# Kernel tuning notes

Measured on AMD Instinct MI355X. Metric: run time of the kernel, lower is better.

The kernel has to match this reference:

```python
import jax, jax.numpy as jnp
import numpy as np

WINDOW = 16
VD = 6
HID = 16


def setup_inputs() -> dict:
    key = jax.random.key(0)
    ks = jax.random.split(key, 10)
    B, S = 256, 4096
    sc = 0.1
    return {
        "x": jax.random.normal(ks[0], (B, S, 2), jnp.float32),
        "h_0": jnp.zeros((B, HID), jnp.float32),
        "fir_I_w": jax.random.normal(ks[1], (VD, WINDOW), jnp.float32) * sc,
        "fir_Q_w": jax.random.normal(ks[2], (VD, WINDOW), jnp.float32) * sc,
        "W_fi_w": jax.random.normal(ks[3], (HID, 2 * VD), jnp.float32) * sc,
        "W_fi_b": jnp.zeros((HID,), jnp.float32),
        "W_fh_w": jax.random.normal(ks[4], (HID, HID), jnp.float32) * sc,
        "W_gi_w": jax.random.normal(ks[5], (HID, 2 * VD), jnp.float32) * sc,
        "W_gi_b": jnp.zeros((HID,), jnp.float32),
        "W_gh_w": jax.random.normal(ks[6], (HID, HID), jnp.float32) * sc,
        "W_out_I_w": jax.random.normal(ks[7], (1, HID), jnp.float32) * sc,
        "W_out_I_b": jnp.zeros((1,), jnp.float32),
        "W_out_Q_w": jax.random.normal(ks[8], (1, HID), jnp.float32) * sc,
        "W_out_Q_b": jnp.zeros((1,), jnp.float32),
    }


def _tile_theta(t, hidden):
    # pr_block replication logic for vd_units < hidden <= 3*vd_units cases
    if VD >= hidden:
        return t[..., :hidden]
    elif hidden <= 2 * VD:
        return jnp.concatenate([t, t[..., : hidden - VD]], axis=-1)
    else:
        return jnp.concatenate([t, t, t[..., : hidden - 2 * VD]], axis=-1)


def reference(x, h_0, fir_I_w, fir_Q_w, W_fi_w, W_fi_b, W_fh_w,
              W_gi_w, W_gi_b, W_gh_w, W_out_I_w, W_out_I_b,
              W_out_Q_w, W_out_Q_b):
    B, S, _ = x.shape
    # Causal sliding windows: window at t covers x[t-15 .. t] with zero pad.
    xp = jnp.concatenate([jnp.zeros((B, WINDOW - 1, 2), x.dtype), x], axis=1)
    idx = jnp.arange(S)[:, None] + jnp.arange(WINDOW)[None, :]  # (S, W)
    win = xp[:, idx, :]  # (B, S, W, 2)
    wI, wQ = win[..., 0], win[..., 1]  # (B, S, W)
    # Complex FIR filter
    I_fir = jnp.einsum('bsw,vw->bsv', wI, fir_I_w) - jnp.einsum('bsw,vw->bsv', wQ, fir_Q_w)
    Q_fir = jnp.einsum('bsw,vw->bsv', wI, fir_Q_w) + jnp.einsum('bsw,vw->bsv', wQ, fir_I_w)
    mag = jnp.sqrt(I_fir * I_fir + Q_fir * Q_fir) + 1e-8
    mag2 = mag * mag
    sin_t = Q_fir / mag
    cos_t = I_fir / mag
    # L = stack([mag, mag2], dim=2).view(B, S, 2*VD)
    L = jnp.stack([mag, mag2], axis=2).reshape(B, S, 2 * VD)
    # Precompute input contributions to gates; scan the recurrence.
    fi = jnp.einsum('bsl,hl->bsh', L, W_fi_w) + W_fi_b  # (B,S,H)
    gi = jnp.einsum('bsl,hl->bsh', L, W_gi_w) + W_gi_b

    def step(h, inp):
        fi_t, gi_t = inp
        f = jax.nn.sigmoid(fi_t + h @ W_fh_w.T)
        g = jnp.tanh(gi_t + h @ W_gh_w.T)
        h = f * h + (1.0 - f) * g
        return h, h

    _, h_seq = jax.lax.scan(step, h_0, (fi.transpose(1, 0, 2), gi.transpose(1, 0, 2)))
    h_seq = h_seq.transpose(1, 0, 2)  # (B, S, H)
    hidden = h_seq.shape[-1]
    cos_r = _tile_theta(cos_t, hidden)
    sin_r = _tile_theta(sin_t, hidden)
    I_rot = h_seq * cos_r
    Q_rot = h_seq * sin_r
    oI = I_rot @ W_out_I_w.T + W_out_I_b  # (B,S,1)
    oQ = Q_rot @ W_out_Q_w.T + W_out_Q_b
    out_I = oI - oQ
    out_Q = oQ + oI
    return jnp.concatenate([out_I, out_Q], axis=-1)
```

## Files before the change

### kernel.cpp

```cpp
#include <hip/hip_runtime.h>
#include <stdint.h>

#define DEV __device__ __forceinline__

constexpr int Bb   = 256;
constexpr int Ss   = 4096;
constexpr int HIDN = 16;
constexpr int VDN  = 6;
constexpr int WINN = 16;

constexpr int BPG   = 32;
constexpr int NG    = Bb / BPG;
constexpr int CHUNK = 16;
constexpr int WARM  = 16;
constexpr int NCH   = Ss / CHUNK;
constexpr int NPH   = (CHUNK + WARM) / 4;
constexpr int EPH   = WARM / 4;

constexpr size_t WSL_BYTES = (size_t)NG * Ss * BPG * 16;
constexpr size_t WSC_BYTES = (size_t)NG * Ss * BPG * 24;

typedef __fp16 h2v   __attribute__((ext_vector_type(2)));
typedef __fp16 f16x8 __attribute__((ext_vector_type(8)));
typedef float  f32x16 __attribute__((ext_vector_type(16)));

DEV uint32_t pk16(float a, float b) {
    h2v t = __builtin_amdgcn_cvt_pkrtz(a, b);
    uint32_t u; __builtin_memcpy(&u, &t, 4); return u;
}
DEV void up16(uint32_t u, float& a, float& b) {
    h2v t; __builtin_memcpy(&t, &u, 4);
    a = (float)t[0]; b = (float)t[1];
}
DEV uint32_t sqpk(uint32_t u) {
    h2v t; __builtin_memcpy(&t, &u, 4);
    t = t * t;
    uint32_t r; __builtin_memcpy(&r, &t, 4); return r;
}
DEV f32x16 MF(const uint32_t* a, const uint32_t* b, f32x16 c) {
    f16x8 av, bv;
    __builtin_memcpy(&av, a, 16);
    __builtin_memcpy(&bv, b, 16);
    return __builtin_amdgcn_mfma_f32_32x32x16_f16(av, bv, c, 0, 0, 0);
}

template<int C> DEV int   dpp_i(int v)  { return __builtin_amdgcn_update_dpp(0, v, C, 0xF, 0xF, false); }
template<int C> DEV float dpp_f(float v){ return __int_as_float(dpp_i<C>(__float_as_int(v))); }
#define DPP_ALL(X) X(1,0x121) X(2,0x122) X(3,0x123) X(4,0x124) X(5,0x125) X(6,0x126) X(7,0x127) \
  X(8,0x128) X(9,0x129) X(10,0x12A) X(11,0x12B) X(12,0x12C) X(13,0x12D) X(14,0x12E) X(15,0x12F)

__global__ __launch_bounds__(256, 4) void boja_front(
    const float* __restrict__ x,
    const float* __restrict__ fIw, const float* __restrict__ fQw,
    uint4* __restrict__ wsl, uint2* __restrict__ wsc)
{
    __shared__ __align__(16) uint4 lsl[256];
    const int tid = threadIdx.x;
    const int tq  = tid & 7;
    const int b_  = tid >> 3;
    const int G   = blockIdx.y;
    const int t0  = blockIdx.x * 8;
    const int t   = t0 + tq;
    const int b   = G * BPG + b_;
    const int id  = b * Ss + t;
    const float2* x2 = (const float2*)x;

    float wI[WINN], wQ[WINN];
    if (t >= WINN - 1) {
#pragma unroll
        for (int w = 0; w < WINN; ++w) { float2 v = x2[id - 15 + w]; wI[w] = v.x; wQ[w] = v.y; }
    } else {
#pragma unroll
        for (int w = 0; w < WINN; ++w) {
            int ts = t - 15 + w;
            float2 v = (ts >= 0) ? x2[id - 15 + w] : make_float2(0.f, 0.f);
            wI[w] = v.x; wQ[w] = v.y;
        }
    }
    float aI[VDN], aQ[VDN];
#pragma unroll
    for (int v = 0; v < VDN; ++v) { aI[v] = 0.f; aQ[v] = 0.f; }
#pragma unroll
    for (int w = 0; w < WINN; ++w) {
#pragma unroll
        for (int v = 0; v < VDN; ++v) {
            aI[v] = fmaf( wI[w], fIw[v*16+w], aI[v]);
            aI[v] = fmaf(-wQ[w], fQw[v*16+w], aI[v]);
            aQ[v] = fmaf( wI[w], fQw[v*16+w], aQ[v]);
            aQ[v] = fmaf( wQ[w], fIw[v*16+w], aQ[v]);
        }
    }
    float mg[VDN];
    uint32_t sc[VDN];
#pragma unroll
    for (int v = 0; v < VDN; ++v) {
        float m2 = fmaf(aI[v], aI[v], aQ[v]*aQ[v]);
        mg[v] = __builtin_amdgcn_sqrtf(m2) + 1e-8f;
        float iv = __builtin_amdgcn_rcpf(mg[v]);
        sc[v] = pk16(aI[v]*iv, aQ[v]*iv);
    }
    {
        const size_t cb = ((size_t)(G * Ss + t) * BPG + b_) * 3;
        wsc[cb+0] = make_uint2(sc[0], sc[1]);
        wsc[cb+1] = make_uint2(sc[2], sc[3]);
        wsc[cb+2] = make_uint2(sc[4], sc[5]);
    }
    lsl[tq*32 + b_] = make_uint4(pk16(mg[0], mg[1]), pk16(mg[2], mg[3]),
                                 pk16(mg[4], mg[5]), pk16(mg[0]*mg[0], mg[1]*mg[1]));
    __syncthreads();
    {
        const int tq2 = tid >> 5, b2 = tid & 31;
        wsl[((size_t)(G*Ss + t0 + tq2)) * BPG + b2] = lsl[tid];
    }
}

__global__ __launch_bounds__(64, 2) void boja_rnn(
    const uint4* __restrict__ wsl, const uint2* __restrict__ wsc,
    const float* __restrict__ h0,
    const float* __restrict__ Wfh, const float* __restrict__ Wgh,
    const float* __restrict__ Wfi, const float* __restrict__ bfi,
    const float* __restrict__ Wgi, const float* __restrict__ bgi,
    const float* __restrict__ WoI, const float* __restrict__ boI,
    const float* __restrict__ WoQ, const float* __restrict__ boQ,
    float* __restrict__ out)
{
    const int l  = threadIdx.x;
    const int b_ = l & 31;
    const int h_ = l >> 5;
    const int G  = blockIdx.x & (NG - 1);
    const int ci = blockIdx.x >> 3;

    const int t_out0  = ci * CHUNK;
    const int t_start = t_out0 - WARM;
    const bool useh0  = (t_start <= 0);

    const float CF = -1.4426950408889634f;
    const float CG =  2.8853900817779268f;
    const int   m  = b_;
    const float sA = (m < 16) ? CF : CG;

    uint32_t a1[4], a2[4];
#pragma unroll
    for (int d = 0; d < 4; ++d) {
        float wv[2], uv[2];
#pragma unroll
        for (int q = 0; q < 2; ++q) {
            const int e = d*2 + q;
            const int k = (e & 3) + 8*(e >> 2) + 4*h_;
            wv[q] = ((m < 16) ? Wfh[m*16 + k] : Wgh[(m-16)*16 + k]) * sA;
            float u;
            if (k < 12)       u = ((m < 16) ? Wfi[m*12 + k] : Wgi[(m-16)*12 + k]) * sA;
            else if (k == 12) u = ((m < 16) ? bfi[m] : bgi[m-16]) * sA;
            else              u = 0.0f;
            uv[q] = u;
        }
        a1[d] = pk16(wv[0], wv[1]);
        a2[d] = pk16(uv[0], uv[1]);
    }

    float woi[8], woq[8];
#pragma unroll
    for (int r = 0; r < 8; ++r) {
        const int j = (r & 3) + 8*(r >> 2) + 4*h_;
        woi[r] = WoI[j]; woq[r] = WoQ[j];
    }
    const float bo_i = boI[0], bo_q = boQ[0];

    float h0r[8];
    if (useh0) {
        const float* hp = h0 + (size_t)(G*BPG + b_) * HIDN;
        float4 p = *(const float4*)(hp + 4*h_);
        float4 q = *(const float4*)(hp + 8 + 4*h_);
        h0r[0]=p.x; h0r[1]=p.y; h0r[2]=p.z; h0r[3]=p.w;
        h0r[4]=q.x; h0r[5]=q.y; h0r[6]=q.z; h0r[7]=q.w;
    }
    float hreg[8];
#pragma unroll
    for (int r = 0; r < 8; ++r) hreg[r] = 0.0f;
    uint32_t b1[4];
    b1[0]=0u; b1[1]=0u; b1[2]=0u; b1[3]=0u;

    f32x16 zero16;
#pragma unroll
    for (int i = 0; i < 16; ++i) zero16[i] = 0.0f;

    const uint4* lp = wsl + (size_t)G * Ss * BPG + b_;
    const uint2* cp = wsc + ((size_t)G * Ss * BPG + b_) * 3;
    float2* outp = (float2*)out + (size_t)(G*BPG + b_) * Ss;

    uint4 LB[3][4];
    uint2 CB[2][4][3];

    auto loadL = [&](uint4 (&B)[4], int tb) {
#pragma unroll
        for (int s = 0; s < 4; ++s) {
            int tq2 = tb + s; tq2 = (tq2 < 0) ? 0 : tq2;
            B[s] = lp[(size_t)tq2 * BPG];
        }
    };
    auto loadC = [&](uint2 (&C)[4][3], int tb) {
#pragma unroll
        for (int s = 0; s < 4; ++s)
#pragma unroll
            for (int k = 0; k < 3; ++k)
                C[s][k] = cp[(size_t)(tb + s) * (BPG*3) + k];
    };

    loadL(LB[0], t_start);
    loadL(LB[1], t_start + 4);

#define PHASE(P) { \
    const int tb = t_start + 4*(P); \
    if ((P) + 2 < NPH) loadL(LB[((P)+2)%3], t_start + 4*((P)+2)); \
    if ((P) + 1 >= EPH && (P) + 1 < NPH) loadC(CB[((P)+1)&1], t_start + 4*((P)+1)); \
    float ob[8]; \
    uint32_t fw[4][4]; \
    _Pragma("unroll") \
    for (int s = 0; s < 4; ++s) { \
        uint4 v = LB[(P)%3][s]; \
        fw[s][0] = h_ ? v.z : v.x; \
        fw[s][1] = h_ ? v.w : v.y; \
        fw[s][2] = h_ ? 0x00003C00u : sqpk(v.y); \
        fw[s][3] = h_ ? 0u : sqpk(v.z); \
    } \
    f32x16 accL = MF(a2, fw[0], zero16); \
    _Pragma("unroll") \
    for (int s = 0; s < 4; ++s) { \
        if (useh0 && tb + s == 0) { \
            _Pragma("unroll") for (int r = 0; r < 8; ++r) hreg[r] = h0r[r]; \
            b1[0]=pk16(hreg[0],hreg[1]); b1[1]=pk16(hreg[2],hreg[3]); \
            b1[2]=pk16(hreg[4],hreg[5]); b1[3]=pk16(hreg[6],hreg[7]); \
        } \
        f32x16 acc = MF(a1, b1, accL); \
        if (s < 3) accL = MF(a2, fw[s+1], zero16); \
        _Pragma("unroll") \
        for (int r = 0; r < 8; ++r) { \
            float f = __builtin_amdgcn_rcpf(1.0f + __builtin_amdgcn_exp2f(acc[r])); \
            float g = fmaf(-2.0f, __builtin_amdgcn_rcpf(1.0f + __builtin_amdgcn_exp2f(acc[r+8])), 1.0f); \
            hreg[r] = fmaf(f, hreg[r] - g, g); \
        } \
        b1[0]=pk16(hreg[0],hreg[1]); b1[1]=pk16(hreg[2],hreg[3]); \
        b1[2]=pk16(hreg[4],hreg[5]); b1[3]=pk16(hreg[6],hreg[7]); \
        if ((P) >= EPH) { \
            float cs6[6], sn6[6]; \
            up16(CB[(P)&1][s][0].x, cs6[0], sn6[0]); up16(CB[(P)&1][s][0].y, cs6[1], sn6[1]); \
            up16(CB[(P)&1][s][1].x, cs6[2], sn6[2]); up16(CB[(P)&1][s][1].y, cs6[3], sn6[3]); \
            up16(CB[(P)&1][s][2].x, cs6[4], sn6[4]); up16(CB[(P)&1][s][2].y, cs6[5], sn6[5]); \
            float oI = bo_i, oQ = bo_q; \
            const bool hb = (h_ != 0); \
            { \
                float c0,sn0; \
                c0 = hb?cs6[4]:cs6[0]; sn0 = hb?sn6[4]:sn6[0]; oI = fmaf(hreg[0]*c0, woi[0], oI); oQ = fmaf(hreg[0]*sn0, woq[0], oQ); \
                c0 = hb?cs6[5]:cs6[1]; sn0 = hb?sn6[5]:sn6[1]; oI = fmaf(hreg[1]*c0, woi[1], oI); oQ = fmaf(hreg[1]*sn0, woq[1], oQ); \
                c0 = hb?cs6[0]:cs6[2]; sn0 = hb?sn6[0]:sn6[2]; oI = fmaf(hreg[2]*c0, woi[2], oI); oQ = fmaf(hreg[2]*sn0, woq[2], oQ); \
                c0 = hb?cs6[1]:cs6[3]; sn0 = hb?sn6[1]:sn6[3]; oI = fmaf(hreg[3]*c0, woi[3], oI); oQ = fmaf(hreg[3]*sn0, woq[3], oQ); \
                c0 = hb?cs6[0]:cs6[2]; sn0 = hb?sn6[0]:sn6[2]; oI = fmaf(hreg[4]*c0, woi[4], oI); oQ = fmaf(hreg[4]*sn0, woq[4], oQ); \
                c0 = hb?cs6[1]:cs6[3]; sn0 = hb?sn6[1]:sn6[3]; oI = fmaf(hreg[5]*c0, woi[5], oI); oQ = fmaf(hreg[5]*sn0, woq[5], oQ); \
                c0 = hb?cs6[2]:cs6[4]; sn0 = hb?sn6[2]:sn6[4]; oI = fmaf(hreg[6]*c0, woi[6], oI); oQ = fmaf(hreg[6]*sn0, woq[6], oQ); \
                c0 = hb?cs6[3]:cs6[5]; sn0 = hb?sn6[3]:sn6[5]; oI = fmaf(hreg[7]*c0, woi[7], oI); oQ = fmaf(hreg[7]*sn0, woq[7], oQ); \
            } \
            oI += __shfl_xor(oI, 32, 64); \
            oQ += __shfl_xor(oQ, 32, 64); \
            ob[s*2] = oI - oQ; ob[s*2+1] = oI + oQ; \
        } \
    } \
    if ((P) >= EPH && l < 32) { \
        float4* po = (float4*)(outp + tb); \
        po[0] = make_float4(ob[0], ob[1], ob[2], ob[3]); \
        po[1] = make_float4(ob[4], ob[5], ob[6], ob[7]); \
    } \
}

    PHASE(0)  PHASE(1)  PHASE(2)  PHASE(3)
    PHASE(4)  PHASE(5)  PHASE(6)  PHASE(7)
#undef PHASE
}

__global__ __launch_bounds__(64, 2) void bojanet_v2(
    const float* __restrict__ x,   const float* __restrict__ h0,
    const float* __restrict__ fIw, const float* __restrict__ fQw,
    const float* __restrict__ Wfi, const float* __restrict__ bfi,
    const float* __restrict__ Wfh, const float* __restrict__ Wgi,
    const float* __restrict__ bgi, const float* __restrict__ Wgh,
    const float* __restrict__ WoI, const float* __restrict__ boI,
    const float* __restrict__ WoQ, const float* __restrict__ boQ,
    float* __restrict__ out)
{
    constexpr int FCH = 128, FWR = 64, FSB = 16;
    __shared__ __align__(16) float s_fi[FSB * 80];
    __shared__ __align__(16) float s_gi[FSB * 80];
    __shared__ __align__(16) float s_h [FSB * 68];
    __shared__ float s_sc[4 * 12 * 17];

    const int lane = threadIdx.x;
    const int j  = lane & 15;
    const int bl = lane >> 4;
    const int ci = blockIdx.x;
    const int b0 = blockIdx.y * 4;
    const int t_out0  = ci * FCH;
    const int t_start = ci ? (t_out0 - FWR) : 0;
    const int t_end   = t_out0 + FCH;

    int c[16]; c[0] = j;
#define CSET(K,CTL) c[K] = dpp_i<CTL>(j);
    DPP_ALL(CSET)
#undef CSET
    float wf[16], wg[16];
#pragma unroll
    for (int k = 0; k < 16; ++k) { wf[k] = Wfh[j*16 + c[k]]; wg[k] = Wgh[j*16 + c[k]]; }

    float h = (ci == 0) ? h0[(b0 + bl) * HIDN + j] : 0.0f;
    const float2* x2   = (const float2*)x + (size_t)(b0 + bl) * Ss;
    float2*       out2 = (float2*)out     + (size_t)(b0 + bl) * Ss;

    for (int tb = t_start; tb < t_end; tb += FSB) {
        const bool emit = (tb >= t_out0);
        {
            const int tg = tb + j;
            float wI[WINN], wQ[WINN];
            if (tb >= WINN - 1) {
#pragma unroll
                for (int w = 0; w < WINN; ++w) { float2 v = x2[tg - 15 + w]; wI[w] = v.x; wQ[w] = v.y; }
            } else {
#pragma unroll
                for (int w = 0; w < WINN; ++w) {
                    int ts = tg - 15 + w;
                    float2 v = (ts >= 0) ? x2[ts] : make_float2(0.f, 0.f);
                    wI[w] = v.x; wQ[w] = v.y;
                }
            }
            float aI[VDN], aQ[VDN];
#pragma unroll
            for (int v = 0; v < VDN; ++v) { aI[v] = 0.f; aQ[v] = 0.f; }
#pragma unroll
            for (int w = 0; w < WINN; ++w) {
#pragma unroll
                for (int v = 0; v < VDN; ++v) {
                    aI[v] = fmaf( wI[w], fIw[v*16+w], aI[v]);
                    aI[v] = fmaf(-wQ[w], fQw[v*16+w], aI[v]);
                    aQ[v] = fmaf( wI[w], fQw[v*16+w], aQ[v]);
                    aQ[v] = fmaf( wQ[w], fIw[v*16+w], aQ[v]);
                }
            }
            float L[12];
#pragma unroll
            for (int v = 0; v < VDN; ++v) {
                float m2 = fmaf(aI[v], aI[v], aQ[v]*aQ[v]);
                float mg = __builtin_amdgcn_sqrtf(m2) + 1e-8f;
                L[v] = mg; L[6+v] = mg*mg;
                if (emit) {
                    float iv = __builtin_amdgcn_rcpf(mg);
                    s_sc[(bl*12 + v  )*17 + j] = aI[v] * iv;
                    s_sc[(bl*12 + 6+v)*17 + j] = aQ[v] * iv;
                }
            }
            float fi[16], gi[16];
#pragma unroll
            for (int k = 0; k < 16; ++k) { fi[k] = bfi[k]; gi[k] = bgi[k]; }
#pragma unroll
            for (int ll = 0; ll < 12; ++ll) {
#pragma unroll
                for (int k = 0; k < 16; ++k) {
                    fi[k] = fmaf(L[ll], Wfi[k*12+ll], fi[k]);
                    gi[k] = fmaf(L[ll], Wgi[k*12+ll], gi[k]);
                }
            }
            float* pf = &s_fi[j*80 + bl*20];
            float* pg = &s_gi[j*80 + bl*20];
#pragma unroll
            for (int qq = 0; qq < 4; ++qq) {
                *(float4*)(pf + 4*qq) = make_float4(fi[4*qq], fi[4*qq+1], fi[4*qq+2], fi[4*qq+3]);
                *(float4*)(pg + 4*qq) = make_float4(gi[4*qq], gi[4*qq+1], gi[4*qq+2], gi[4*qq+3]);
            }
        }
        __asm__ volatile("s_waitcnt lgkmcnt(0)" ::: "memory");
        {
            const int rb = bl*20 + j;
            float pf0 = s_fi[rb], pf1 = s_fi[80 + rb];
            float pg0 = s_gi[rb], pg1 = s_gi[80 + rb];
#pragma unroll
            for (int tt = 0; tt < FSB; ++tt) {
                const int nx = (tt + 2 < FSB) ? tt + 2 : FSB - 1;
                float pfn = s_fi[nx*80 + rb];
                float pgn = s_gi[nx*80 + rb];
                float hr[16]; hr[0] = h;
#define HSET(K,CTL) hr[K] = dpp_f<CTL>(h);
                DPP_ALL(HSET)
#undef HSET
                float af0 = pf0, af1 = 0.f, ag0 = pg0, ag1 = 0.f;
#pragma unroll
                for (int k = 0; k < 8; ++k) {
                    af0 = fmaf(wf[k],   hr[k],   af0);
                    ag0 = fmaf(wg[k],   hr[k],   ag0);
                    af1 = fmaf(wf[k+8], hr[k+8], af1);
                    ag1 = fmaf(wg[k+8], hr[k+8], ag1);
                }
                float zf = af0 + af1, zg = ag0 + ag1;
                float f = __builtin_amdgcn_rcpf(1.0f + __builtin_amdgcn_exp2f(zf * -1.4426950408889634f));
                float g = fmaf(-2.0f, __builtin_amdgcn_rcpf(1.0f + __builtin_amdgcn_exp2f(zg * 2.8853900817779268f)), 1.0f);
                h = fmaf(f, h - g, g);
                s_h[tt*68 + bl*16 + j] = h;
                pf0 = pf1; pf1 = pfn; pg0 = pg1; pg1 = pgn;
            }
        }
        __asm__ volatile("s_waitcnt lgkmcnt(0)" ::: "memory");
        if (emit) {
            const int tg = tb + j;
            float hv[16];
#pragma unroll
            for (int qq = 0; qq < 4; ++qq) {
                float4 t4 = *(const float4*)&s_h[j*68 + bl*16 + 4*qq];
                hv[4*qq] = t4.x; hv[4*qq+1] = t4.y; hv[4*qq+2] = t4.z; hv[4*qq+3] = t4.w;
            }
            float cs[12];
#pragma unroll
            for (int k = 0; k < 12; ++k) cs[k] = s_sc[(bl*12 + k)*17 + j];
            float oI = boI[0], oQ = boQ[0];
#pragma unroll
            for (int k = 0; k < 16; ++k) {
                int v = (k < 6) ? k : ((k < 12) ? k - 6 : k - 12);
                oI = fmaf(hv[k]*cs[v],   WoI[k], oI);
                oQ = fmaf(hv[k]*cs[6+v], WoQ[k], oQ);
            }
            out2[tg] = make_float2(oI - oQ, oI + oQ);
        }
        __asm__ volatile("s_waitcnt lgkmcnt(0)" ::: "memory");
    }
}

extern "C" void kernel_launch(void* const* d_in, const int* in_sizes, int n_in,
                              void* d_out, int out_size, void* d_ws, size_t ws_size,
                              hipStream_t stream) {
    const float* x   = (const float*)d_in[0];
    const float* h0  = (const float*)d_in[1];
    const float* fIw = (const float*)d_in[2];
    const float* fQw = (const float*)d_in[3];
    const float* Wfi = (const float*)d_in[4];
    const float* bfi = (const float*)d_in[5];
    const float* Wfh = (const float*)d_in[6];
    const float* Wgi = (const float*)d_in[7];
    const float* bgi = (const float*)d_in[8];
    const float* Wgh = (const float*)d_in[9];
    const float* WoI = (const float*)d_in[10];
    const float* boI = (const float*)d_in[11];
    const float* WoQ = (const float*)d_in[12];
    const float* boQ = (const float*)d_in[13];
    float* out = (float*)d_out;

    if (ws_size >= WSL_BYTES + WSC_BYTES) {
        uint4* wsl = (uint4*)d_ws;
        uint2* wsc = (uint2*)((char*)d_ws + WSL_BYTES);
        boja_front<<<dim3(Ss/8, NG), 256, 0, stream>>>(x, fIw, fQw, wsl, wsc);
        boja_rnn<<<dim3(NG * NCH), 64, 0, stream>>>(
            wsl, wsc, h0, Wfh, Wgh, Wfi, bfi, Wgi, bgi, WoI, boI, WoQ, boQ, out);
    } else {
        bojanet_v2<<<dim3(32, Bb / 4), 64, 0, stream>>>(
            x, h0, fIw, fQw, Wfi, bfi, Wfh, Wgi, bgi, Wgh, WoI, boI, WoQ, boQ, out);
    }
}
```

Baseline: 50.91 us.

## Stage RNN chunk inputs into LDS via async global_load_lds with vmcnt waits

The front kernel's cos/sin workspace layout changes to a planar per-timestep arrangement with three 256-byte planes. The RNN kernel now issues all loads for its chunk up front using global_load_lds DMA into shared memory, replacing the register-based triple/double buffering. Each phase waits on a hand-computed vmcnt before reading from LDS, so compute can start while later loads are still in flight. This adds 28KB of LDS per block, which can limit occupancy, and relies on the hard-coded vmcnt counts matching the order in which loads are issued.

```diff
diff --git a/kernel.cpp b/kernel.cpp
--- a/kernel.cpp
+++ b/kernel.cpp
@@ -42,6 +42,13 @@
     __builtin_memcpy(&av, a, 16);
     __builtin_memcpy(&bv, b, 16);
     return __builtin_amdgcn_mfma_f32_32x32x16_f16(av, bv, c, 0, 0, 0);
+}
+
+DEV void gl_lds16(const uint8_t* g, uint8_t* l) {
+    __builtin_amdgcn_global_load_lds(
+        (const __attribute__((address_space(1))) uint32_t*)g,
+        (__attribute__((address_space(3))) uint32_t*)l, 16, 0, 0);
+    asm volatile("" ::: "memory");
 }
 
 template<int C> DEV int   dpp_i(int v)  { return __builtin_amdgcn_update_dpp(0, v, C, 0xF, 0xF, false); }
@@ -100,10 +107,10 @@
         sc[v] = pk16(aI[v]*iv, aQ[v]*iv);
     }
     {
-        const size_t cb = ((size_t)(G * Ss + t) * BPG + b_) * 3;
-        wsc[cb+0] = make_uint2(sc[0], sc[1]);
-        wsc[cb+1] = make_uint2(sc[2], sc[3]);
-        wsc[cb+2] = make_uint2(sc[4], sc[5]);
+        const size_t cb = ((size_t)(G * Ss + t)) * 96;
+        wsc[cb +  0 + b_] = make_uint2(sc[0], sc[1]);
+        wsc[cb + 32 + b_] = make_uint2(sc[2], sc[3]);
+        wsc[cb + 64 + b_] = make_uint2(sc[4], sc[5]);
     }
     lsl[tq*32 + b_] = make_uint4(pk16(mg[0], mg[1]), pk16(mg[2], mg[3]),
                                  pk16(mg[4], mg[5]), pk16(mg[0]*mg[0], mg[1]*mg[1]));
@@ -124,6 +131,8 @@
     const float* __restrict__ WoQ, const float* __restrict__ boQ,
     float* __restrict__ out)
 {
+    __shared__ __align__(1024) uint8_t sbuf[28672];
+
     const int l  = threadIdx.x;
     const int b_ = l & 31;
     const int h_ = l >> 5;
@@ -184,46 +193,37 @@
 #pragma unroll
     for (int i = 0; i < 16; ++i) zero16[i] = 0.0f;
 
-    const uint4* lp = wsl + (size_t)G * Ss * BPG + b_;
-    const uint2* cp = wsc + ((size_t)G * Ss * BPG + b_) * 3;
+    {
+        asm volatile("" ::: "memory");
+        const uint8_t* wb = (const uint8_t*)wsl + (size_t)G * Ss * 512;
+#pragma unroll
+        for (int i = 0; i < 16; ++i) {
+            int t = t_start + 2*i + h_;
+            t = (t < 0) ? 0 : t;
+            gl_lds16(wb + (size_t)t * 512 + b_ * 16, sbuf + i * 1024);
+        }
+        const uint8_t* wc = (const uint8_t*)wsc + ((size_t)G * Ss + t_out0) * 768 + l * 16;
+#pragma unroll
+        for (int j = 0; j < 12; ++j)
+            gl_lds16(wc + j * 1024, sbuf + 16384 + j * 1024);
+    }
+
     float2* outp = (float2*)out + (size_t)(G*BPG + b_) * Ss;
 
-    uint4 LB[3][4];
-    uint2 CB[2][4][3];
-
-    auto loadL = [&](uint4 (&B)[4], int tb) {
-#pragma unroll
-        for (int s = 0; s < 4; ++s) {
-            int tq2 = tb + s; tq2 = (tq2 < 0) ? 0 : tq2;
-            B[s] = lp[(size_t)tq2 * BPG];
-        }
-    };
-    auto loadC = [&](uint2 (&C)[4][3], int tb) {
-#pragma unroll
-        for (int s = 0; s < 4; ++s)
-#pragma unroll
-            for (int k = 0; k < 3; ++k)
-                C[s][k] = cp[(size_t)(tb + s) * (BPG*3) + k];
-    };
-
-    loadL(LB[0], t_start);
-    loadL(LB[1], t_start + 4);
-
-#define PHASE(P) { \
+#define PHASE(P, NW) { \
+    asm volatile("s_waitcnt vmcnt(" #NW ")" ::: "memory"); \
     const int tb = t_start + 4*(P); \
-    if ((P) + 2 < NPH) loadL(LB[((P)+2)%3], t_start + 4*((P)+2)); \
-    if ((P) + 1 >= EPH && (P) + 1 < NPH) loadC(CB[((P)+1)&1], t_start + 4*((P)+1)); \
-    float ob[8]; \
     uint32_t fw[4][4]; \
     _Pragma("unroll") \
     for (int s = 0; s < 4; ++s) { \
-        uint4 v = LB[(P)%3][s]; \
+        uint4 v = *(const uint4*)(sbuf + (4*(P)+s)*512 + b_*16); \
         fw[s][0] = h_ ? v.z : v.x; \
         fw[s][1] = h_ ? v.w : v.y; \
         fw[s][2] = h_ ? 0x00003C00u : sqpk(v.y); \
         fw[s][3] = h_ ? 0u : sqpk(v.z); \
     } \
     f32x16 accL = MF(a2, fw[0], zero16); \
+    float ob[8]; \
     _Pragma("unroll") \
     for (int s = 0; s < 4; ++s) { \
         if (useh0 && tb + s == 0) { \
@@ -242,22 +242,26 @@
         b1[0]=pk16(hreg[0],hreg[1]); b1[1]=pk16(hreg[2],hreg[3]); \
         b1[2]=pk16(hreg[4],hreg[5]); b1[3]=pk16(hreg[6],hreg[7]); \
         if ((P) >= EPH) { \
+            const uint8_t* cbp = sbuf + 16384 + (4*((P)-EPH)+s)*768 + b_*8; \
+            uint2 c0 = *(const uint2*)(cbp); \
+            uint2 c1 = *(const uint2*)(cbp + 256); \
+            uint2 c2 = *(const uint2*)(cbp + 512); \
             float cs6[6], sn6[6]; \
-            up16(CB[(P)&1][s][0].x, cs6[0], sn6[0]); up16(CB[(P)&1][s][0].y, cs6[1], sn6[1]); \
-            up16(CB[(P)&1][s][1].x, cs6[2], sn6[2]); up16(CB[(P)&1][s][1].y, cs6[3], sn6[3]); \
-            up16(CB[(P)&1][s][2].x, cs6[4], sn6[4]); up16(CB[(P)&1][s][2].y, cs6[5], sn6[5]); \
+            up16(c0.x, cs6[0], sn6[0]); up16(c0.y, cs6[1], sn6[1]); \
+            up16(c1.x, cs6[2], sn6[2]); up16(c1.y, cs6[3], sn6[3]); \
+            up16(c2.x, cs6[4], sn6[4]); up16(c2.y, cs6[5], sn6[5]); \
             float oI = bo_i, oQ = bo_q; \
             const bool hb = (h_ != 0); \
             { \
-                float c0,sn0; \
-                c0 = hb?cs6[4]:cs6[0]; sn0 = hb?sn6[4]:sn6[0]; oI = fmaf(hreg[0]*c0, woi[0], oI); oQ = fmaf(hreg[0]*sn0, woq[0], oQ); \
-                c0 = hb?cs6[5]:cs6[1]; sn0 = hb?sn6[5]:sn6[1]; oI = fmaf(hreg[1]*c0, woi[1], oI); oQ = fmaf(hreg[1]*sn0, woq[1], oQ); \
-                c0 = hb?cs6[0]:cs6[2]; sn0 = hb?sn6[0]:sn6[2]; oI = fmaf(hreg[2]*c0, woi[2], oI); oQ = fmaf(hreg[2]*sn0, woq[2], oQ); \
-                c0 = hb?cs6[1]:cs6[3]; sn0 = hb?sn6[1]:sn6[3]; oI = fmaf(hreg[3]*c0, woi[3], oI); oQ = fmaf(hreg[3]*sn0, woq[3], oQ); \
-                c0 = hb?cs6[0]:cs6[2]; sn0 = hb?sn6[0]:sn6[2]; oI = fmaf(hreg[4]*c0, woi[4], oI); oQ = fmaf(hreg[4]*sn0, woq[4], oQ); \
-                c0 = hb?cs6[1]:cs6[3]; sn0 = hb?sn6[1]:sn6[3]; oI = fmaf(hreg[5]*c0, woi[5], oI); oQ = fmaf(hreg[5]*sn0, woq[5], oQ); \
-                c0 = hb?cs6[2]:cs6[4]; sn0 = hb?sn6[2]:sn6[4]; oI = fmaf(hreg[6]*c0, woi[6], oI); oQ = fmaf(hreg[6]*sn0, woq[6], oQ); \
-                c0 = hb?cs6[3]:cs6[5]; sn0 = hb?sn6[3]:sn6[5]; oI = fmaf(hreg[7]*c0, woi[7], oI); oQ = fmaf(hreg[7]*sn0, woq[7], oQ); \
+                float c0f,sn0; \
+                c0f = hb?cs6[4]:cs6[0]; sn0 = hb?sn6[4]:sn6[0]; oI = fmaf(hreg[0]*c0f, woi[0], oI); oQ = fmaf(hreg[0]*sn0, woq[0], oQ); \
+                c0f = hb?cs6[5]:cs6[1]; sn0 = hb?sn6[5]:sn6[1]; oI = fmaf(hreg[1]*c0f, woi[1], oI); oQ = fmaf(hreg[1]*sn0, woq[1], oQ); \
+                c0f = hb?cs6[0]:cs6[2]; sn0 = hb?sn6[0]:sn6[2]; oI = fmaf(hreg[2]*c0f, woi[2], oI); oQ = fmaf(hreg[2]*sn0, woq[2], oQ); \
+                c0f = hb?cs6[1]:cs6[3]; sn0 = hb?sn6[1]:sn6[3]; oI = fmaf(hreg[3]*c0f, woi[3], oI); oQ = fmaf(hreg[3]*sn0, woq[3], oQ); \
+                c0f = hb?cs6[0]:cs6[2]; sn0 = hb?sn6[0]:sn6[2]; oI = fmaf(hreg[4]*c0f, woi[4], oI); oQ = fmaf(hreg[4]*sn0, woq[4], oQ); \
+                c0f = hb?cs6[1]:cs6[3]; sn0 = hb?sn6[1]:sn6[3]; oI = fmaf(hreg[5]*c0f, woi[5], oI); oQ = fmaf(hreg[5]*sn0, woq[5], oQ); \
+                c0f = hb?cs6[2]:cs6[4]; sn0 = hb?sn6[2]:sn6[4]; oI = fmaf(hreg[6]*c0f, woi[6], oI); oQ = fmaf(hreg[6]*sn0, woq[6], oQ); \
+                c0f = hb?cs6[3]:cs6[5]; sn0 = hb?sn6[3]:sn6[5]; oI = fmaf(hreg[7]*c0f, woi[7], oI); oQ = fmaf(hreg[7]*sn0, woq[7], oQ); \
             } \
             oI += __shfl_xor(oI, 32, 64); \
             oQ += __shfl_xor(oQ, 32, 64); \
@@ -271,8 +275,8 @@
     } \
 }
 
-    PHASE(0)  PHASE(1)  PHASE(2)  PHASE(3)
-    PHASE(4)  PHASE(5)  PHASE(6)  PHASE(7)
+    PHASE(0,26) PHASE(1,24) PHASE(2,22) PHASE(3,20)
+    PHASE(4,9)  PHASE(5,8)  PHASE(6,7)  PHASE(7,6)
 #undef PHASE
 }
 
```

Result: slower. 64.48 us (+26.7%).
